# Kernel optimization log

Hardware: AMD Instinct MI355X
Metric: run time of the kernel (lower is better)

## Reference

```python
import jax, jax.numpy as jnp
import numpy as np

N = 100000   # nodes
E = 1600000  # edges
F = 128      # in = hidden channels
L = 4        # num GCN layers
G = 512      # graphs in batch
OUT = 10     # classes
EPS = 1e-5


def setup_inputs() -> dict:
    key = jax.random.key(0)
    ks = jax.random.split(key, 12)
    x = jax.random.normal(ks[0], (N, F), dtype=jnp.float32)
    edge_index = jax.random.randint(ks[1], (2, E), 0, N, dtype=jnp.int64)
    batch = jnp.sort(jax.random.randint(ks[2], (N,), 0, G, dtype=jnp.int64))
    s = 1.0 / np.sqrt(F)
    Ws = jax.random.uniform(ks[3], (L, F, F), jnp.float32, -s, s)
    bs = jax.random.uniform(ks[4], (L, F), jnp.float32, -s, s)
    gammas = jnp.ones((L, F), jnp.float32)
    betas = jnp.zeros((L, F), jnp.float32)
    s1 = 1.0 / np.sqrt(F * L)
    W1 = jax.random.uniform(ks[5], (F * L, F), jnp.float32, -s1, s1)
    b1 = jax.random.uniform(ks[6], (F,), jnp.float32, -s1, s1)
    g1 = jnp.ones((F,), jnp.float32)
    bt1 = jnp.zeros((F,), jnp.float32)
    s2 = 1.0 / np.sqrt(F)
    W2 = jax.random.uniform(ks[7], (F, OUT), jnp.float32, -s2, s2)
    b2 = jax.random.uniform(ks[8], (OUT,), jnp.float32, -s2, s2)
    return {"x": x, "edge_index": edge_index, "batch": batch, "Ws": Ws, "bs": bs,
            "gammas": gammas, "betas": betas, "W1": W1, "b1": b1, "g1": g1,
            "bt1": bt1, "W2": W2, "b2": b2}


def _batch_norm(x, g, b):
    # training-mode BatchNorm1d over the node dim (biased variance)
    mu = jnp.mean(x, axis=0)
    var = jnp.var(x, axis=0)
    return (x - mu) * jax.lax.rsqrt(var + EPS) * g + b


def reference(x, edge_index, batch, Ws, bs, gammas, betas, W1, b1, g1, bt1, W2, b2):
    row, col = edge_index[0], edge_index[1]
    # GCN normalization (add_self_loops=False since normalize=True)
    deg = jax.ops.segment_sum(jnp.ones((E,), x.dtype), col, num_segments=N)
    dinv = jnp.where(deg > 0, jax.lax.rsqrt(deg), 0.0)
    norm = dinv[row] * dinv[col]  # [E]
    pooled = []
    h = x
    for t in range(L):
        hw = h @ Ws[t]                                    # [N, F]
        msg = norm[:, None] * hw[row]                     # gather  [E, F]
        h = jax.ops.segment_sum(msg, col, num_segments=N) + bs[t]  # scatter [N, F]
        h = jax.nn.relu(h)
        h = _batch_norm(h, gammas[t], betas[t])
        pooled.append(jax.ops.segment_sum(h, batch, num_segments=G))  # [G, F]
    z = jnp.concatenate(pooled, axis=1)                   # [G, L*F]
    z = z @ W1 + b1
    z = _batch_norm(z, g1, bt1)
    z = jax.nn.relu(z)
    return z @ W2 + b2                                    # [G, OUT]
```

## Files before the change

kernel.cpp:

```cpp
#include <hip/hip_runtime.h>

#define NN 100000
#define EE 1600000
#define FF 128
#define LL 4
#define GG 512
#define OUTC 10
#define EPSF 1e-5f
#define NSCB ((NN + 255) / 256)

#define NPW 16
#define AGG_WAVES ((NN + NPW - 1) / NPW)
#define AGG_BLOCKS ((AGG_WAVES + 3) / 4)

typedef __attribute__((ext_vector_type(8))) short short8;
typedef __attribute__((ext_vector_type(4))) float f32x4;

__device__ inline unsigned bf16rne(float f) {
  unsigned u = __float_as_uint(f);
  return (u + 0x7fffu + ((u >> 16) & 1u)) >> 16;
}
__device__ inline unsigned packbf(float lo, float hi) {
  return bf16rne(lo) | (bf16rne(hi) << 16);
}
__device__ inline float bflo(unsigned u) { return __uint_as_float(u << 16); }
__device__ inline float bfhi(unsigned u) { return __uint_as_float(u & 0xffff0000u); }


__global__ __launch_bounds__(256) void k_deg(const int* __restrict__ col, int* __restrict__ deg) {
  int e = blockIdx.x * 256 + threadIdx.x;
  if (e < EE) atomicAdd(&deg[col[e]], 1);
}

__global__ __launch_bounds__(256) void k_bsum(const int* __restrict__ deg,
                                              int* __restrict__ bsum,
                                              float* __restrict__ dinv) {
  int i = blockIdx.x * 256 + threadIdx.x;
  int v = (i < NN) ? deg[i] : 0;
  if (i < NN) dinv[i] = v > 0 ? rsqrtf((float)v) : 0.0f;
#pragma unroll
  for (int off = 32; off > 0; off >>= 1) v += __shfl_down(v, off, 64);
  __shared__ int ws[4];
  if ((threadIdx.x & 63) == 0) ws[threadIdx.x >> 6] = v;
  __syncthreads();
  if (threadIdx.x == 0) bsum[blockIdx.x] = ws[0] + ws[1] + ws[2] + ws[3];
}

__global__ __launch_bounds__(256) void k_rowptr(const int* __restrict__ deg,
                                                const int* __restrict__ bsum,
                                                int* __restrict__ rowptr) {
  __shared__ int sb[512];
  __shared__ int sd[256];
  const int t = threadIdx.x;
  sb[t]       = (t < NSCB) ? bsum[t] : 0;
  sb[t + 256] = (t + 256 < NSCB) ? bsum[t + 256] : 0;
  __syncthreads();
#pragma unroll
  for (int off = 1; off < 512; off <<= 1) {
    int v0 = (t >= off) ? sb[t - off] : 0;
    int v1 = sb[t + 256 - off];
    __syncthreads();
    sb[t] += v0;
    sb[t + 256] += v1;
    __syncthreads();
  }
  const int bpre = (blockIdx.x == 0) ? 0 : sb[blockIdx.x - 1];
  const int i = blockIdx.x * 256 + t;
  const int d = (i < NN) ? deg[i] : 0;
  sd[t] = d;
  __syncthreads();
#pragma unroll
  for (int off = 1; off < 256; off <<= 1) {
    int v = (t >= off) ? sd[t - off] : 0;
    __syncthreads();
    sd[t] += v;
    __syncthreads();
  }
  if (i < NN) rowptr[i] = bpre + sd[t] - d;
  if (blockIdx.x == 0 && t == 0) rowptr[NN] = EE;
}

__global__ __launch_bounds__(256) void k_fill(const int* __restrict__ ei,
                                              const int* __restrict__ rowptr,
                                              int* __restrict__ cnt,
                                              const float* __restrict__ dinv,
                                              int2* __restrict__ ecw) {
  int e = blockIdx.x * 256 + threadIdx.x;
  if (e >= EE) return;
  int r = ei[e];
  int cl = ei[EE + e];
  int slot = rowptr[cl] + atomicAdd(&cnt[cl], 1);
  ecw[slot] = make_int2(r, __float_as_int(dinv[r] * dinv[cl]));
}


__global__ __launch_bounds__(256) void k_cvt(const float* __restrict__ x,
                                             const int* __restrict__ batch,
                                             unsigned* __restrict__ Ab,
                                             int* __restrict__ gstart) {
  int i = blockIdx.x * 256 + threadIdx.x;
  if (i < NN * 64) {
    float2 v = *(const float2*)(x + (size_t)i * 2);
    Ab[i] = packbf(v.x, v.y);
  }
  if (i < NN) {
    int b = batch[i];
    if (i == 0) {
      for (int g = 0; g <= b; ++g) gstart[g] = 0;
    } else {
      int bp = batch[i - 1];
      for (int g = bp + 1; g <= b; ++g) gstart[g] = i;
    }
    if (i == NN - 1) {
      for (int g = b + 1; g <= GG; ++g) gstart[g] = NN;
    }
  }
}

__global__ __launch_bounds__(256) void k_wcvt(const float* __restrict__ W,
                                              uint4* __restrict__ Wf) {
  int tid = blockIdx.x * 256 + threadIdx.x;
  int lane = tid & 63;
  int which = (tid >> 6) & 1;
  int ct = (tid >> 7) & 7;
  int kc = tid >> 10;
  int n = ct * 16 + (lane & 15);
  int k0 = kc * 32 + (lane >> 4) * 8;
  unsigned h[8];
#pragma unroll
  for (int j = 0; j < 8; ++j) {
    float w = W[(k0 + j) * 128 + n];
    unsigned hb = bf16rne(w);
    if (which == 0) {
      h[j] = hb;
    } else {
      float hf = __uint_as_float(hb << 16);
      h[j] = bf16rne(w - hf);
    }
  }
  uint4 o;
  o.x = h[0] | (h[1] << 16);
  o.y = h[2] | (h[3] << 16);
  o.z = h[4] | (h[5] << 16);
  o.w = h[6] | (h[7] << 16);
  Wf[tid] = o;
}

__global__ __launch_bounds__(256) void k_post(const float* __restrict__ bnbuf,
                                              const float* __restrict__ gamma,
                                              const float* __restrict__ beta,
                                              float* __restrict__ bnsc,
                                              const float* __restrict__ Wnext,
                                              uint4* __restrict__ Wf,
                                              float* __restrict__ baseo) {
  __shared__ float ssc[256];
  const int t = threadIdx.x;
  if (t < 128) {
    float mu = bnbuf[t] * (1.0f / NN);
    float var = bnbuf[128 + t] * (1.0f / NN) - mu * mu;
    float inv = rsqrtf(var + EPSF);
    float sc = gamma[t] * inv;
    float sh = beta[t] - mu * sc;
    ssc[t] = sc;
    ssc[128 + t] = sh;
    if (blockIdx.x == 0) {
      bnsc[t] = sc;
      bnsc[128 + t] = sh;
    }
  }
  __syncthreads();
  if (gridDim.x == 1) return;
  if (blockIdx.x < 16) {
    int tid = blockIdx.x * 256 + t;
    int lane = tid & 63;
    int which = (tid >> 6) & 1;
    int ct = (tid >> 7) & 7;
    int kc = tid >> 10;
    int n = ct * 16 + (lane & 15);
    int k0 = kc * 32 + (lane >> 4) * 8;
    unsigned h[8];
#pragma unroll
    for (int j = 0; j < 8; ++j) {
      float w = Wnext[(k0 + j) * 128 + n] * ssc[k0 + j];
      unsigned hb = bf16rne(w);
      if (which == 0) {
        h[j] = hb;
      } else {
        float hf = __uint_as_float(hb << 16);
        h[j] = bf16rne(w - hf);
      }
    }
    uint4 o;
    o.x = h[0] | (h[1] << 16);
    o.y = h[2] | (h[3] << 16);
    o.z = h[4] | (h[5] << 16);
    o.w = h[6] | (h[7] << 16);
    Wf[tid] = o;
  } else if (t < 128) {
    float acc = 0.f;
    for (int k = 0; k < 128; ++k) acc = fmaf(ssc[128 + k], Wnext[k * 128 + t], acc);
    baseo[t] = acc;
  }
}

__global__ __launch_bounds__(256) void k_mm(const unsigned* __restrict__ Ab,
                                            const uint4* __restrict__ Wf,
                                            unsigned* __restrict__ Bb) {
  const int lane = threadIdx.x & 63;
  const int w = threadIdx.x >> 6;
  const int quad = lane >> 4;
  const int m = lane & 15;
  const int rowbase = blockIdx.x * 64 + w * 16;
  const int arow = min(rowbase + m, NN - 1);
  const uint4* A4 = (const uint4*)Ab;
  f32x4 acc[8];
#pragma unroll
  for (int ct = 0; ct < 8; ++ct) acc[ct] = (f32x4){0.f, 0.f, 0.f, 0.f};
#pragma unroll
  for (int kc = 0; kc < 4; ++kc) {
    uint4 av = A4[arow * 16 + kc * 4 + quad];
    short8 af = *(short8*)&av;
#pragma unroll
    for (int ct = 0; ct < 8; ++ct) {
      uint4 bh = Wf[((kc * 8 + ct) * 2 + 0) * 64 + lane];
      uint4 bl = Wf[((kc * 8 + ct) * 2 + 1) * 64 + lane];
      acc[ct] = __builtin_amdgcn_mfma_f32_16x16x32_bf16(af, *(short8*)&bh, acc[ct], 0, 0, 0);
      acc[ct] = __builtin_amdgcn_mfma_f32_16x16x32_bf16(af, *(short8*)&bl, acc[ct], 0, 0, 0);
    }
  }
#pragma unroll
  for (int ct = 0; ct < 8; ++ct) {
#pragma unroll
    for (int r = 0; r < 4; ++r) {
      float v = acc[ct][r];
      float vo = __shfl_xor(v, 1);
      int row = rowbase + quad * 4 + r;
      if ((lane & 1) == 0 && row < NN) {
        Bb[row * 64 + ct * 8 + (m >> 1)] = packbf(v, vo);
      }
    }
  }
}

__global__ __launch_bounds__(256) void k_agg(const unsigned* __restrict__ Bb,
                                             const int* __restrict__ rowptr,
                                             const int2* __restrict__ ecw,
                                             const float* __restrict__ bias,
                                             const float* __restrict__ base,
                                             const int* __restrict__ batch,
                                             unsigned* __restrict__ Ar,
                                             float* __restrict__ bnbuf,
                                             float* __restrict__ pooledt) {
  const int lane = threadIdx.x & 63;
  const int wave = threadIdx.x >> 6;
  const int c = lane * 2;
  const int gwave = blockIdx.x * 4 + wave;
  const int n0 = gwave * NPW;
  const float2 bv = *(const float2*)(bias + c);
  const float2 basev = *(const float2*)(base + c);
  float s0 = 0.f, s1 = 0.f, q0 = 0.f, q1 = 0.f;
  __shared__ int srp[4][NPW + 1];
  __shared__ int2 sstage[4][64];
  if (n0 < NN) {
    const int nn = min(NPW, NN - n0);
    if (lane <= nn) srp[wave][lane] = rowptr[n0 + lane];
    int bsp = (lane < nn) ? batch[n0 + lane] : 0;
    float ax0 = 0.f, ax1 = 0.f, ay0 = 0.f, ay1 = 0.f, sw = 0.f;
    float px = 0.f, py = 0.f;
    int gprev = -1;
    auto finalize = [&](int node) {
      float rx = fmaxf(fmaf(sw, basev.x, ax0 + ax1) + bv.x, 0.f);
      float ry = fmaxf(fmaf(sw, basev.y, ay0 + ay1) + bv.y, 0.f);
      Ar[(size_t)(n0 + node) * 64 + lane] = packbf(rx, ry);
      s0 += rx; s1 += ry;
      q0 = fmaf(rx, rx, q0); q1 = fmaf(ry, ry, q1);
      int g = __shfl(bsp, node);
      if (g != gprev) {
        if (gprev >= 0) {
          atomicAdd(&pooledt[(size_t)gprev * 512 + c], px);
          atomicAdd(&pooledt[(size_t)gprev * 512 + c + 1], py);
        }
        gprev = g; px = 0.f; py = 0.f;
      }
      px += rx; py += ry;
      ax0 = 0.f; ax1 = 0.f; ay0 = 0.f; ay1 = 0.f; sw = 0.f;
    };
    const int beg = __builtin_amdgcn_readfirstlane(srp[wave][0]);
    const int endall = __builtin_amdgcn_readfirstlane(srp[wave][nn]);
    int cn = 0;
    while (cn < nn && __builtin_amdgcn_readfirstlane(srp[wave][cn + 1]) == beg) {
      finalize(cn);
      ++cn;
    }
    int nend = (cn < nn) ? __builtin_amdgcn_readfirstlane(srp[wave][cn + 1]) : 0x7fffffff;
    int2 stage = (beg + lane < endall) ? ecw[beg + lane] : make_int2(0, 0);
    for (int base_e = beg; base_e < endall; base_e += 64) {
      sstage[wave][lane] = stage;
      const int nb = base_e + 64;
      if (nb < endall) {
        stage = (nb + lane < endall) ? ecw[nb + lane] : make_int2(0, 0);
      }
#pragma unroll
      for (int g = 0; g < 4; ++g) {
        if (base_e + g * 16 < endall) {
          int2 ew[16]; unsigned us[16];
#pragma unroll
          for (int j = 0; j < 16; ++j) ew[j] = sstage[wave][g * 16 + j];
#pragma unroll
          for (int j = 0; j < 16; ++j) {
            const int sj = __builtin_amdgcn_readfirstlane(ew[j].x);
            us[j] = Bb[((size_t)(unsigned)sj << 6) + (unsigned)lane];
          }
#pragma unroll
          for (int j = 0; j < 16; ++j) {
            const float wj = __int_as_float(ew[j].y);
            sw += wj;
            if (j & 1) {
              ax1 = fmaf(wj, bflo(us[j]), ax1);
              ay1 = fmaf(wj, bfhi(us[j]), ay1);
            } else {
              ax0 = fmaf(wj, bflo(us[j]), ax0);
              ay0 = fmaf(wj, bfhi(us[j]), ay0);
            }
            const int e1 = base_e + g * 16 + j + 1;
            if (e1 == nend) {
              finalize(cn);
              ++cn;
              nend = (cn < nn) ? __builtin_amdgcn_readfirstlane(srp[wave][cn + 1]) : 0x7fffffff;
              while (cn < nn && nend == e1) {
                finalize(cn);
                ++cn;
                nend = (cn < nn) ? __builtin_amdgcn_readfirstlane(srp[wave][cn + 1]) : 0x7fffffff;
              }
            }
          }
        }
      }
    }
    if (gprev >= 0) {
      atomicAdd(&pooledt[(size_t)gprev * 512 + c], px);
      atomicAdd(&pooledt[(size_t)gprev * 512 + c + 1], py);
    }
  }
  __shared__ float sred[4][256];
  sred[wave][c] = s0;
  sred[wave][c + 1] = s1;
  sred[wave][128 + c] = q0;
  sred[wave][128 + c + 1] = q1;
  __syncthreads();
  const int t = threadIdx.x;
  float tot = sred[0][t] + sred[1][t] + sred[2][t] + sred[3][t];
  atomicAdd(&bnbuf[t], tot);
}


__global__ __launch_bounds__(128) void k_z1(const float* __restrict__ S,
                                            const float* __restrict__ bnscL,
                                            const int* __restrict__ gstart,
                                            const float* __restrict__ W1,
                                            const float* __restrict__ b1,
                                            float* __restrict__ z1) {
  __shared__ float sp[512];
  const int g = blockIdx.x;
  const float cntg = (float)(gstart[g + 1] - gstart[g]);
  for (int i = threadIdx.x; i < 512; i += 128) {
    int t = i >> 7, ch = i & 127;
    sp[i] = fmaf(bnscL[t * 256 + ch], S[(size_t)g * 512 + i], cntg * bnscL[t * 256 + 128 + ch]);
  }
  __syncthreads();
  const int c = threadIdx.x;
  float acc = b1[c];
  for (int j = 0; j < 512; ++j) acc = fmaf(sp[j], W1[j * 128 + c], acc);
  z1[(size_t)g * 128 + c] = acc;
}

__global__ __launch_bounds__(1024) void k_zstat(const float* __restrict__ z1,
                                                const float* __restrict__ g1,
                                                const float* __restrict__ bt1,
                                                float* __restrict__ zsc) {
  const int t = threadIdx.x;
  const int c = t & 127;
  const int gr = t >> 7;
  float s = 0.f, q = 0.f;
  for (int g = gr; g < GG; g += 8) {
    float v = z1[(size_t)g * 128 + c];
    s += v;
    q = fmaf(v, v, q);
  }
  __shared__ float ss[8][128];
  __shared__ float sq[8][128];
  ss[gr][c] = s;
  sq[gr][c] = q;
  __syncthreads();
  if (t < 128) {
    float st = 0.f, qt = 0.f;
#pragma unroll
    for (int i = 0; i < 8; ++i) { st += ss[i][c]; qt += sq[i][c]; }
    float mu = st * (1.0f / GG);
    float var = qt * (1.0f / GG) - mu * mu;
    float inv = rsqrtf(var + EPSF);
    float sc = g1[c] * inv;
    zsc[c] = sc;
    zsc[128 + c] = bt1[c] - mu * sc;
  }
}

__global__ __launch_bounds__(128) void k_out(const float* __restrict__ z1,
                                             const float* __restrict__ zsc,
                                             const float* __restrict__ W2,
                                             const float* __restrict__ b2,
                                             float* __restrict__ out) {
  __shared__ float zr[128];
  const int g = blockIdx.x;
  const int c = threadIdx.x;
  zr[c] = fmaxf(fmaf(z1[(size_t)g * 128 + c], zsc[c], zsc[128 + c]), 0.f);
  __syncthreads();
  if (c < OUTC) {
    float acc = b2[c];
    for (int k = 0; k < 128; ++k) acc = fmaf(zr[k], W2[k * OUTC + c], acc);
    out[(size_t)g * OUTC + c] = acc;
  }
}


extern "C" void kernel_launch(void* const* d_in, const int* in_sizes, int n_in,
                              void* d_out, int out_size, void* d_ws, size_t ws_size,
                              hipStream_t stream) {
  const float* x      = (const float*)d_in[0];
  const int*   ei     = (const int*)d_in[1];
  const int*   batch  = (const int*)d_in[2];
  const float* Ws     = (const float*)d_in[3];
  const float* bs     = (const float*)d_in[4];
  const float* gammas = (const float*)d_in[5];
  const float* betas  = (const float*)d_in[6];
  const float* W1     = (const float*)d_in[7];
  const float* b1     = (const float*)d_in[8];
  const float* g1     = (const float*)d_in[9];
  const float* bt1    = (const float*)d_in[10];
  const float* W2     = (const float*)d_in[11];
  const float* b2     = (const float*)d_in[12];
  float* out = (float*)d_out;

  char* ws = (char*)d_ws;
  size_t off = 0;
  auto alloc = [&](size_t bytes) -> void* {
    void* p = ws + off;
    off = (off + bytes + 255) & ~(size_t)255;
    return p;
  };
  int*   deg    = (int*)alloc((size_t)NN * 4);
  int*   cnt    = (int*)alloc((size_t)NN * 4);
  float* bnbuf  = (float*)alloc((size_t)LL * 256 * 4);
  float* pooled = (float*)alloc((size_t)GG * 512 * 4);
  float* zbase  = (float*)alloc(128 * 4);
  size_t zero_bytes = off;
  unsigned* Ar     = (unsigned*)alloc((size_t)NN * 64 * 4);
  unsigned* Ab     = (unsigned*)alloc((size_t)NN * 64 * 4);
  unsigned* Bb     = (unsigned*)alloc((size_t)NN * 64 * 4);
  int2*     ecw    = (int2*)alloc((size_t)EE * 8);
  float*    dinv   = (float*)alloc((size_t)NN * 4);
  int*      rowptr = (int*)alloc((size_t)(NN + 1) * 4);
  int*      bsum   = (int*)alloc((size_t)NSCB * 4);
  int*      gstart = (int*)alloc((size_t)(GG + 1) * 4);
  uint4*    Wf     = (uint4*)alloc((size_t)4096 * 16);
  float*    z1     = (float*)alloc((size_t)GG * FF * 4);
  float*    bnscL  = (float*)alloc((size_t)LL * 256 * 4);
  float*    basebf = (float*)alloc(128 * 4);
  float*    zsc    = (float*)alloc(256 * 4);
  (void)ws_size; (void)in_sizes; (void)n_in; (void)out_size;

  hipMemsetAsync(d_ws, 0, zero_bytes, stream);

  k_deg<<<(EE + 255) / 256, 256, 0, stream>>>(ei + EE, deg);
  k_bsum<<<NSCB, 256, 0, stream>>>(deg, bsum, dinv);
  k_rowptr<<<NSCB, 256, 0, stream>>>(deg, bsum, rowptr);
  k_fill<<<(EE + 255) / 256, 256, 0, stream>>>(ei, rowptr, cnt, dinv, ecw);
  k_cvt<<<(NN * 64 + 255) / 256, 256, 0, stream>>>(x, batch, Ab, gstart);
  k_wcvt<<<16, 256, 0, stream>>>(Ws, Wf);

  for (int t = 0; t < LL; ++t) {
    k_mm<<<(NN + 63) / 64, 256, 0, stream>>>(t == 0 ? Ab : Ar, Wf, Bb);
    k_agg<<<AGG_BLOCKS, 256, 0, stream>>>(Bb, rowptr, ecw, bs + t * FF,
                                          t == 0 ? zbase : basebf, batch,
                                          Ar, bnbuf + t * 256, pooled + t * FF);
    if (t < LL - 1) {
      k_post<<<17, 256, 0, stream>>>(bnbuf + t * 256, gammas + t * FF, betas + t * FF,
                                     bnscL + t * 256, Ws + (size_t)(t + 1) * 16384,
                                     Wf, basebf);
    } else {
      k_post<<<1, 256, 0, stream>>>(bnbuf + t * 256, gammas + t * FF, betas + t * FF,
                                    bnscL + t * 256, nullptr, nullptr, nullptr);
    }
  }

  k_z1<<<GG, 128, 0, stream>>>(pooled, bnscL, gstart, W1, b1, z1);
  k_zstat<<<1, 1024, 0, stream>>>(z1, g1, bt1, zsc);
  k_out<<<GG, 128, 0, stream>>>(z1, zsc, W2, b2, out);
}
```

Measured before the change: 781.3 us.

## Fuse BN-stat post step into aggregation tail, widen matmul and z1 tiles

Removes the separate k_post launch per layer. The last aggregation block, detected with an atomic counter plus thread fences, now computes the BN scale and shift, folds the scale into the next layer's bf16 split weights, and computes the base vector. Separately, k_mm now handles 32 rows per wave so each loaded weight fragment feeds two MFMA row tiles, and k_z1 processes four graphs per block so W1 loads are shared. Costs are a serial tail done by one block in the aggregation kernel and higher register use in k_mm.

New measurement: 1.388 ms. 77.6% more time.

```diff
diff --git a/kernel.cpp b/kernel.cpp
--- a/kernel.cpp
+++ b/kernel.cpp
@@ -146,63 +146,6 @@
   Wf[tid] = o;
 }
 
-__global__ __launch_bounds__(256) void k_post(const float* __restrict__ bnbuf,
-                                              const float* __restrict__ gamma,
-                                              const float* __restrict__ beta,
-                                              float* __restrict__ bnsc,
-                                              const float* __restrict__ Wnext,
-                                              uint4* __restrict__ Wf,
-                                              float* __restrict__ baseo) {
-  __shared__ float ssc[256];
-  const int t = threadIdx.x;
-  if (t < 128) {
-    float mu = bnbuf[t] * (1.0f / NN);
-    float var = bnbuf[128 + t] * (1.0f / NN) - mu * mu;
-    float inv = rsqrtf(var + EPSF);
-    float sc = gamma[t] * inv;
-    float sh = beta[t] - mu * sc;
-    ssc[t] = sc;
-    ssc[128 + t] = sh;
-    if (blockIdx.x == 0) {
-      bnsc[t] = sc;
-      bnsc[128 + t] = sh;
-    }
-  }
-  __syncthreads();
-  if (gridDim.x == 1) return;
-  if (blockIdx.x < 16) {
-    int tid = blockIdx.x * 256 + t;
-    int lane = tid & 63;
-    int which = (tid >> 6) & 1;
-    int ct = (tid >> 7) & 7;
-    int kc = tid >> 10;
-    int n = ct * 16 + (lane & 15);
-    int k0 = kc * 32 + (lane >> 4) * 8;
-    unsigned h[8];
-#pragma unroll
-    for (int j = 0; j < 8; ++j) {
-      float w = Wnext[(k0 + j) * 128 + n] * ssc[k0 + j];
-      unsigned hb = bf16rne(w);
-      if (which == 0) {
-        h[j] = hb;
-      } else {
-        float hf = __uint_as_float(hb << 16);
-        h[j] = bf16rne(w - hf);
-      }
-    }
-    uint4 o;
-    o.x = h[0] | (h[1] << 16);
-    o.y = h[2] | (h[3] << 16);
-    o.z = h[4] | (h[5] << 16);
-    o.w = h[6] | (h[7] << 16);
-    Wf[tid] = o;
-  } else if (t < 128) {
-    float acc = 0.f;
-    for (int k = 0; k < 128; ++k) acc = fmaf(ssc[128 + k], Wnext[k * 128 + t], acc);
-    baseo[t] = acc;
-  }
-}
-
 __global__ __launch_bounds__(256) void k_mm(const unsigned* __restrict__ Ab,
                                             const uint4* __restrict__ Wf,
                                             unsigned* __restrict__ Bb) {
@@ -210,33 +153,45 @@
   const int w = threadIdx.x >> 6;
   const int quad = lane >> 4;
   const int m = lane & 15;
-  const int rowbase = blockIdx.x * 64 + w * 16;
-  const int arow = min(rowbase + m, NN - 1);
+  const int rowbase = blockIdx.x * 128 + w * 32;
+  const int arow0 = min(rowbase + m, NN - 1);
+  const int arow1 = min(rowbase + 16 + m, NN - 1);
   const uint4* A4 = (const uint4*)Ab;
-  f32x4 acc[8];
-#pragma unroll
-  for (int ct = 0; ct < 8; ++ct) acc[ct] = (f32x4){0.f, 0.f, 0.f, 0.f};
+  f32x4 acc[2][8];
+#pragma unroll
+  for (int rf = 0; rf < 2; ++rf)
+#pragma unroll
+    for (int ct = 0; ct < 8; ++ct) acc[rf][ct] = (f32x4){0.f, 0.f, 0.f, 0.f};
 #pragma unroll
   for (int kc = 0; kc < 4; ++kc) {
-    uint4 av = A4[arow * 16 + kc * 4 + quad];
-    short8 af = *(short8*)&av;
+    uint4 av0 = A4[arow0 * 16 + kc * 4 + quad];
+    uint4 av1 = A4[arow1 * 16 + kc * 4 + quad];
+    short8 af0 = *(short8*)&av0;
+    short8 af1 = *(short8*)&av1;
 #pragma unroll
     for (int ct = 0; ct < 8; ++ct) {
       uint4 bh = Wf[((kc * 8 + ct) * 2 + 0) * 64 + lane];
       uint4 bl = Wf[((kc * 8 + ct) * 2 + 1) * 64 + lane];
-      acc[ct] = __builtin_amdgcn_mfma_f32_16x16x32_bf16(af, *(short8*)&bh, acc[ct], 0, 0, 0);
-      acc[ct] = __builtin_amdgcn_mfma_f32_16x16x32_bf16(af, *(short8*)&bl, acc[ct], 0, 0, 0);
-    }
-  }
-#pragma unroll
-  for (int ct = 0; ct < 8; ++ct) {
-#pragma unroll
-    for (int r = 0; r < 4; ++r) {
-      float v = acc[ct][r];
-      float vo = __shfl_xor(v, 1);
-      int row = rowbase + quad * 4 + r;
-      if ((lane & 1) == 0 && row < NN) {
-        Bb[row * 64 + ct * 8 + (m >> 1)] = packbf(v, vo);
+      short8 bhf = *(short8*)&bh;
+      short8 blf = *(short8*)&bl;
+      acc[0][ct] = __builtin_amdgcn_mfma_f32_16x16x32_bf16(af0, bhf, acc[0][ct], 0, 0, 0);
+      acc[0][ct] = __builtin_amdgcn_mfma_f32_16x16x32_bf16(af0, blf, acc[0][ct], 0, 0, 0);
+      acc[1][ct] = __builtin_amdgcn_mfma_f32_16x16x32_bf16(af1, bhf, acc[1][ct], 0, 0, 0);
+      acc[1][ct] = __builtin_amdgcn_mfma_f32_16x16x32_bf16(af1, blf, acc[1][ct], 0, 0, 0);
+    }
+  }
+#pragma unroll
+  for (int rf = 0; rf < 2; ++rf) {
+#pragma unroll
+    for (int ct = 0; ct < 8; ++ct) {
+#pragma unroll
+      for (int r = 0; r < 4; ++r) {
+        float v = acc[rf][ct][r];
+        float vo = __shfl_xor(v, 1);
+        int row = rowbase + rf * 16 + quad * 4 + r;
+        if ((lane & 1) == 0 && row < NN) {
+          Bb[row * 64 + ct * 8 + (m >> 1)] = packbf(v, vo);
+        }
       }
     }
   }
@@ -250,7 +205,14 @@
                                              const int* __restrict__ batch,
                                              unsigned* __restrict__ Ar,
                                              float* __restrict__ bnbuf,
-                                             float* __restrict__ pooledt) {
+                                             float* __restrict__ pooledt,
+                                             const float* __restrict__ gamma,
+                                             const float* __restrict__ beta,
+                                             float* __restrict__ bnsc,
+                                             const float* __restrict__ Wnext,
+                                             uint4* __restrict__ Wf,
+                                             float* __restrict__ baseo,
+                                             unsigned* __restrict__ ctr) {
   const int lane = threadIdx.x & 63;
   const int wave = threadIdx.x >> 6;
   const int c = lane * 2;
@@ -351,6 +313,61 @@
   const int t = threadIdx.x;
   float tot = sred[0][t] + sred[1][t] + sred[2][t] + sred[3][t];
   atomicAdd(&bnbuf[t], tot);
+
+  __threadfence();
+  __syncthreads();
+  __shared__ int lastf;
+  if (t == 0) lastf = (atomicAdd(ctr, 1u) == (unsigned)(gridDim.x - 1));
+  __syncthreads();
+  if (!lastf) return;
+  __threadfence();
+  __shared__ float ssc[256];
+  if (t < 128) {
+    float mu = bnbuf[t] * (1.0f / NN);
+    float var = bnbuf[128 + t] * (1.0f / NN) - mu * mu;
+    float inv = rsqrtf(var + EPSF);
+    float sc = gamma[t] * inv;
+    float sh = beta[t] - mu * sc;
+    ssc[t] = sc;
+    ssc[128 + t] = sh;
+    bnsc[t] = sc;
+    bnsc[128 + t] = sh;
+  }
+  __syncthreads();
+  if (!Wnext) return;
+#pragma unroll
+  for (int i = 0; i < 16; ++i) {
+    int tid = t + i * 256;
+    int lane2 = tid & 63;
+    int which = (tid >> 6) & 1;
+    int ct = (tid >> 7) & 7;
+    int kc = tid >> 10;
+    int n = ct * 16 + (lane2 & 15);
+    int k0 = kc * 32 + (lane2 >> 4) * 8;
+    unsigned h[8];
+#pragma unroll
+    for (int j = 0; j < 8; ++j) {
+      float w = Wnext[(k0 + j) * 128 + n] * ssc[k0 + j];
+      unsigned hb = bf16rne(w);
+      if (which == 0) {
+        h[j] = hb;
+      } else {
+        float hf = __uint_as_float(hb << 16);
+        h[j] = bf16rne(w - hf);
+      }
+    }
+    uint4 o;
+    o.x = h[0] | (h[1] << 16);
+    o.y = h[2] | (h[3] << 16);
+    o.z = h[4] | (h[5] << 16);
+    o.w = h[6] | (h[7] << 16);
+    Wf[tid] = o;
+  }
+  if (t < 128) {
+    float acc = 0.f;
+    for (int k = 0; k < 128; ++k) acc = fmaf(ssc[128 + k], Wnext[k * 128 + t], acc);
+    baseo[t] = acc;
+  }
 }
 
 
@@ -360,18 +377,32 @@
                                             const float* __restrict__ W1,
                                             const float* __restrict__ b1,
                                             float* __restrict__ z1) {
-  __shared__ float sp[512];
-  const int g = blockIdx.x;
-  const float cntg = (float)(gstart[g + 1] - gstart[g]);
-  for (int i = threadIdx.x; i < 512; i += 128) {
-    int t = i >> 7, ch = i & 127;
-    sp[i] = fmaf(bnscL[t * 256 + ch], S[(size_t)g * 512 + i], cntg * bnscL[t * 256 + 128 + ch]);
-  }
-  __syncthreads();
+  __shared__ float sp[4][512];
+  const int g0 = blockIdx.x * 4;
   const int c = threadIdx.x;
-  float acc = b1[c];
-  for (int j = 0; j < 512; ++j) acc = fmaf(sp[j], W1[j * 128 + c], acc);
-  z1[(size_t)g * 128 + c] = acc;
+#pragma unroll
+  for (int q = 0; q < 4; ++q) {
+    const int g = g0 + q;
+    const float cntg = (float)(gstart[g + 1] - gstart[g]);
+    for (int i = c; i < 512; i += 128) {
+      int tt = i >> 7, ch = i & 127;
+      sp[q][i] = fmaf(bnscL[tt * 256 + ch], S[(size_t)g * 512 + i],
+                      cntg * bnscL[tt * 256 + 128 + ch]);
+    }
+  }
+  __syncthreads();
+  float a0 = b1[c], a1 = a0, a2 = a0, a3 = a0;
+  for (int j = 0; j < 512; ++j) {
+    float w = W1[j * 128 + c];
+    a0 = fmaf(sp[0][j], w, a0);
+    a1 = fmaf(sp[1][j], w, a1);
+    a2 = fmaf(sp[2][j], w, a2);
+    a3 = fmaf(sp[3][j], w, a3);
+  }
+  z1[(size_t)(g0 + 0) * 128 + c] = a0;
+  z1[(size_t)(g0 + 1) * 128 + c] = a1;
+  z1[(size_t)(g0 + 2) * 128 + c] = a2;
+  z1[(size_t)(g0 + 3) * 128 + c] = a3;
 }
 
 __global__ __launch_bounds__(1024) void k_zstat(const float* __restrict__ z1,
@@ -453,6 +484,7 @@
   float* bnbuf  = (float*)alloc((size_t)LL * 256 * 4);
   float* pooled = (float*)alloc((size_t)GG * 512 * 4);
   float* zbase  = (float*)alloc(128 * 4);
+  unsigned* ctr = (unsigned*)alloc((size_t)LL * 4);
   size_t zero_bytes = off;
   unsigned* Ar     = (unsigned*)alloc((size_t)NN * 64 * 4);
   unsigned* Ab     = (unsigned*)alloc((size_t)NN * 64 * 4);
@@ -479,21 +511,15 @@
   k_wcvt<<<16, 256, 0, stream>>>(Ws, Wf);
 
   for (int t = 0; t < LL; ++t) {
-    k_mm<<<(NN + 63) / 64, 256, 0, stream>>>(t == 0 ? Ab : Ar, Wf, Bb);
-    k_agg<<<AGG_BLOCKS, 256, 0, stream>>>(Bb, rowptr, ecw, bs + t * FF,
-                                          t == 0 ? zbase : basebf, batch,
-                                          Ar, bnbuf + t * 256, pooled + t * FF);
-    if (t < LL - 1) {
-      k_post<<<17, 256, 0, stream>>>(bnbuf + t * 256, gammas + t * FF, betas + t * FF,
-                                     bnscL + t * 256, Ws + (size_t)(t + 1) * 16384,
-                                     Wf, basebf);
-    } else {
-      k_post<<<1, 256, 0, stream>>>(bnbuf + t * 256, gammas + t * FF, betas + t * FF,
-                                    bnscL + t * 256, nullptr, nullptr, nullptr);
-    }
-  }
-
-  k_z1<<<GG, 128, 0, stream>>>(pooled, bnscL, gstart, W1, b1, z1);
+    k_mm<<<(NN + 127) / 128, 256, 0, stream>>>(t == 0 ? Ab : Ar, Wf, Bb);
+    k_agg<<<AGG_BLOCKS, 256, 0, stream>>>(
+        Bb, rowptr, ecw, bs + t * FF, t == 0 ? zbase : basebf, batch,
+        Ar, bnbuf + t * 256, pooled + t * FF,
+        gammas + t * FF, betas + t * FF, bnscL + t * 256,
+        t < LL - 1 ? Ws + (size_t)(t + 1) * 16384 : nullptr, Wf, basebf, ctr + t);
+  }
+
+  k_z1<<<GG / 4, 128, 0, stream>>>(pooled, bnscL, gstart, W1, b1, z1);
   k_zstat<<<1, 1024, 0, stream>>>(z1, g1, bt1, zsc);
   k_out<<<GG, 128, 0, stream>>>(z1, zsc, W2, b2, out);
 }
```
